# Performance work log

Measured on AMD Instinct MI355X. Metric: run time of the kernel, lower is better.

## Reference

```python
import jax, jax.numpy as jnp
import numpy as np

B, S, E = 4, 2048, 1024
H, D = 16, 64  # num_heads, attention_head_dim


def setup_inputs() -> dict:
    key = jax.random.key(0)
    ks = jax.random.split(key, 9)
    scale_e = 1.0 / np.sqrt(E)
    scale_hd = 1.0 / np.sqrt(H * D)
    x = jax.random.normal(ks[0], (B, S, E), dtype=jnp.float32)
    # per-head projection weights, stacked: [H, E, D]
    Wq = jax.random.uniform(ks[1], (H, E, D), minval=-scale_e, maxval=scale_e, dtype=jnp.float32)
    Wk = jax.random.uniform(ks[2], (H, E, D), minval=-scale_e, maxval=scale_e, dtype=jnp.float32)
    Wv = jax.random.uniform(ks[3], (H, E, D), minval=-scale_e, maxval=scale_e, dtype=jnp.float32)
    bq = jax.random.uniform(ks[4], (H, D), minval=-scale_e, maxval=scale_e, dtype=jnp.float32)
    bk = jax.random.uniform(ks[5], (H, D), minval=-scale_e, maxval=scale_e, dtype=jnp.float32)
    bv = jax.random.uniform(ks[6], (H, D), minval=-scale_e, maxval=scale_e, dtype=jnp.float32)
    Wo = jax.random.uniform(ks[7], (H * D, E), minval=-scale_hd, maxval=scale_hd, dtype=jnp.float32)
    bo = jax.random.uniform(ks[8], (E,), minval=-scale_hd, maxval=scale_hd, dtype=jnp.float32)
    return {"x": x, "Wq": Wq, "Wk": Wk, "Wv": Wv, "bq": bq, "bk": bk, "bv": bv, "Wo": Wo, "bo": bo}


def reference(x, Wq, Wk, Wv, bq, bk, bv, Wo, bo):
    # Per-head QKV projections, vectorized over heads: [B,H,S,D]
    Q = jnp.einsum('bse,hed->bhsd', x, Wq) + bq[None, :, None, :]
    K = jnp.einsum('bse,hed->bhsd', x, Wk) + bk[None, :, None, :]
    V = jnp.einsum('bse,hed->bhsd', x, Wv) + bv[None, :, None, :]
    scale = 1.0 / jnp.sqrt(jnp.asarray(D, dtype=Q.dtype))
    scores = jnp.einsum('bhsd,bhtd->bhst', Q, K) * scale  # [B,H,S,S]
    attn = jax.nn.softmax(scores, axis=-1)
    Z = jnp.einsum('bhst,bhtd->bhsd', attn, V)            # [B,H,S,D]
    # concat heads on feature dim -> [B,S,H*D], then output projection
    Zc = jnp.transpose(Z, (0, 2, 1, 3)).reshape(B, S, H * D)
    return Zc @ Wo + bo
```

## Files before the change

kernel.cpp:

```cpp
#include <hip/hip_runtime.h>


typedef __attribute__((ext_vector_type(4)))  float   f32x4;
typedef __attribute__((ext_vector_type(16))) float   f32x16;
typedef __attribute__((ext_vector_type(8)))  __bf16  bf16x8;
typedef __attribute__((ext_vector_type(4)))  __bf16  bf16x4;
typedef __attribute__((ext_vector_type(4)))  unsigned int u32x4;
typedef unsigned int u32;

#if __has_builtin(__builtin_amdgcn_exp2f)
#define EXP2F(x) __builtin_amdgcn_exp2f(x)
#else
#define EXP2F(x) exp2f(x)
#endif

__device__ __forceinline__ f32x4 fzero4() {
    f32x4 z = {0.f, 0.f, 0.f, 0.f};
    return z;
}
__device__ __forceinline__ f32x16 fzero16() {
    f32x16 z;
#pragma unroll
    for (int i = 0; i < 16; i++) z[i] = 0.f;
    return z;
}

__device__ __forceinline__ u32 cvtpk_bf16(float lo, float hi_) {
    u32 r;
    asm("v_cvt_pk_bf16_f32 %0, %1, %2" : "=v"(r) : "v"(lo), "v"(hi_));
    return r;
}

__device__ __forceinline__ void gload_lds16(const void* g, void* l) {
    __builtin_amdgcn_global_load_lds(
        (const __attribute__((address_space(1))) u32*)g,
        (__attribute__((address_space(3))) u32*)l, 16, 0, 0);
}

__global__ __launch_bounds__(256) void cvt_f32_bf16_4(
    const float* __restrict__ s, __bf16* __restrict__ d, long n) {
    long i = ((long)blockIdx.x * 256 + threadIdx.x) * 4;
    if (i >= n) return;
    float4 v = *(const float4*)(s + i);
    bf16x4 o = { (__bf16)v.x, (__bf16)v.y, (__bf16)v.z, (__bf16)v.w };
    *(bf16x4*)(d + i) = o;
}

__global__ __launch_bounds__(256) void pack_w_t(
    const float* __restrict__ src, __bf16* __restrict__ dst, int R, int C) {
    __shared__ float t[32][33];
    const int z = blockIdx.z;
    src += (size_t)z * R * C;
    dst += (size_t)z * R * C;
    const int r0 = blockIdx.x * 32, c0 = blockIdx.y * 32;
    const int x = threadIdx.x, y = threadIdx.y;
#pragma unroll
    for (int i = 0; i < 4; i++)
        t[y + i * 8][x] = src[(size_t)(r0 + y + i * 8) * C + c0 + x];
    __syncthreads();
#pragma unroll
    for (int i = 0; i < 4; i++)
        dst[(size_t)(c0 + y + i * 8) * R + r0 + x] = (__bf16)t[x][y + i * 8];
}

__global__ __launch_bounds__(256) void pack_bias(
    const float* __restrict__ bq, const float* __restrict__ bk,
    const float* __restrict__ bv, float* __restrict__ bqkv) {
    int n = blockIdx.x * 256 + threadIdx.x;
    if (n >= 3072) return;
    int t = n >> 10, r = n & 1023;
    const float* s = (t == 0) ? bq : (t == 1) ? bk : bv;
    bqkv[n] = s[r];
}

#define GEMM_STAGE(BUF, KOFF)                                                  \
  {                                                                            \
    gload_lds16(A + arow0 * K + (KOFF) + kcol,                                 \
                (char*)As + (BUF) * 16384 + wid * 1024);                       \
    gload_lds16(A + arow1 * K + (KOFF) + kcol,                                 \
                (char*)As + (BUF) * 16384 + 8192 + wid * 1024);                \
    gload_lds16(Bt + brow * K + (KOFF) + kcol,                                 \
                (char*)Bs + (BUF) * 8192 + wid * 1024);                        \
  }

#define GEMM_COMPUTE(BUF)                                                      \
  {                                                                            \
    bf16x8 a[4], b[4];                                                         \
    _Pragma("unroll")                                                          \
    for (int mi = 0; mi < 4; mi++)                                             \
      a[mi] = *(const bf16x8*)&As[(BUF) * 8192 +                               \
                                  (mr * 64 + mi * 16 + l15) * 32 + l4 * 8];    \
    _Pragma("unroll")                                                          \
    for (int ni = 0; ni < 4; ni++)                                             \
      b[ni] = *(const bf16x8*)&Bs[(BUF) * 4096 +                               \
                                  (nc * 64 + ni * 16 + l15) * 32 + l4 * 8];    \
    _Pragma("unroll")                                                          \
    for (int mi = 0; mi < 4; mi++)                                             \
      _Pragma("unroll")                                                        \
      for (int ni = 0; ni < 4; ni++)                                           \
        acc[mi][ni] = __builtin_amdgcn_mfma_f32_16x16x32_bf16(                 \
            a[mi], b[ni], acc[mi][ni], 0, 0, 0);                               \
  }

#define GEMM_PREAMBLE                                                          \
    const int tid  = threadIdx.x;                                              \
    const int lane = tid & 63, wid = tid >> 6;                                 \
    const int mr = wid >> 1, nc = wid & 1;                                     \
    const int l15 = lane & 15, l4 = lane >> 4;                                 \
    const int bn = blockIdx.x, bm = blockIdx.y;                                \
    const long arow0 = (long)bm * 256 + (tid >> 2);                            \
    const long arow1 = arow0 + 128;                                            \
    const long brow  = (long)bn * 128 + (tid >> 2);                            \
    const int  kcol  = (tid & 3) * 8;                                          \
    f32x4 acc[4][4];                                                           \
    _Pragma("unroll")                                                          \
    for (int i = 0; i < 4; i++)                                                \
      _Pragma("unroll")                                                        \
      for (int j = 0; j < 4; j++) acc[i][j] = fzero4();                        \
    GEMM_STAGE(0, 0)                                                           \
    __syncthreads();                                                           \
    int cur = 0;                                                               \
    for (int k0 = 0; k0 < K; k0 += 32, cur ^= 1) {                             \
        if (k0 + 32 < K) GEMM_STAGE(cur ^ 1, k0 + 32)                          \
        GEMM_COMPUTE(cur)                                                      \
        __syncthreads();                                                       \
    }

template <bool F32OUT>
__global__ __launch_bounds__(512) void gemm_bt(
    const __bf16* __restrict__ A, const __bf16* __restrict__ Bt,
    const float* __restrict__ bias, void* __restrict__ Cout,
    int M, int N, int K, int ldc) {
    __shared__ __bf16 As[2 * 256 * 32];
    __shared__ __bf16 Bs[2 * 128 * 32];
    GEMM_PREAMBLE

#pragma unroll
    for (int mi = 0; mi < 4; mi++)
#pragma unroll
        for (int ni = 0; ni < 4; ni++) {
            const int row = bm * 256 + mr * 64 + mi * 16 + l4 * 4;
            const int col = bn * 128 + nc * 64 + ni * 16 + l15;
            const float bv = bias ? bias[col] : 0.f;
#pragma unroll
            for (int r = 0; r < 4; r++) {
                float v = acc[mi][ni][r] + bv;
                if (F32OUT)
                    ((float*)Cout)[(long)(row + r) * ldc + col] = v;
                else
                    ((__bf16*)Cout)[(long)(row + r) * ldc + col] = (__bf16)v;
            }
        }
}

__global__ __launch_bounds__(512) void gemm_qkv(
    const __bf16* __restrict__ A, const __bf16* __restrict__ Bt,
    const float* __restrict__ bias, __bf16* __restrict__ QKV,
    __bf16* __restrict__ VT, int K) {
    __shared__ __bf16 As[2 * 256 * 32];
    __shared__ __bf16 Bs[2 * 128 * 32];
    GEMM_PREAMBLE

    if (bn < 16) {
#pragma unroll
        for (int mi = 0; mi < 4; mi++)
#pragma unroll
            for (int ni = 0; ni < 4; ni++) {
                const int row = bm * 256 + mr * 64 + mi * 16 + l4 * 4;
                const int col = bn * 128 + nc * 64 + ni * 16 + l15;
                const float bv = bias[col];
#pragma unroll
                for (int r = 0; r < 4; r++)
                    QKV[(long)(row + r) * 3072 + col] =
                        (__bf16)(acc[mi][ni][r] + bv);
            }
    } else {
#pragma unroll
        for (int mi = 0; mi < 4; mi++)
#pragma unroll
            for (int ni = 0; ni < 4; ni++) {
                const int row = bm * 256 + mr * 64 + mi * 16 + l4 * 4;
                const int col = bn * 128 + nc * 64 + ni * 16 + l15;
                const float bv = bias[col];
                const int vcol = col - 2048;
                const int h = vcol >> 6, dcol = vcol & 63;
                const int bb = row >> 11, s = row & 2047;
                bf16x4 o;
#pragma unroll
                for (int r = 0; r < 4; r++)
                    o[r] = (__bf16)(acc[mi][ni][r] + bv);
                *(bf16x4*)&VT[((size_t)(bb * 16 + h) * 64 + dcol) * 2048 + s] = o;
            }
    }
}

__global__ __launch_bounds__(256, 4) void attn_fwd(
    const __bf16* __restrict__ QKV, const __bf16* __restrict__ VT,
    __bf16* __restrict__ Z) {
    const int S = 2048, LDQ = 3072;
    const int dd = blockIdx.x;
    const int blk = (dd & 7) * 128 + (dd >> 3);
    const int qt = blk & 15, bh = blk >> 4, b = bh >> 4, h = bh & 15;
    const int tid = threadIdx.x, wid = tid >> 6, lane = tid & 63;
    const int l31 = lane & 31, hi = lane >> 5;

    __shared__ __bf16 smem[16384];

    const __bf16* Qb = QKV + (size_t)b * S * LDQ + h * 64;
    const __bf16* Kb = Qb + 1024;
    const __bf16* Vb = VT + (size_t)bh * 64 * S;
    const int qrow = qt * 128 + wid * 32;

    bf16x8 qf[4];
#pragma unroll
    for (int kk = 0; kk < 4; kk++)
        qf[kk] = *(const bf16x8*)(Qb + (size_t)(qrow + l31) * LDQ + kk * 16 + hi * 8);

    const int f0 = wid * 2, f1 = wid * 2 + 1;
    const int kr0 = (f0 >> 2) * 32 + l31, kc0 = (f0 & 3) * 16 + hi * 8;
    const int kr1 = (f1 >> 2) * 32 + l31, kc1 = (f1 & 3) * 16 + hi * 8;
    const int vr0 = kr0, vs0 = kc0;
    const int vr1 = kr1, vs1 = kc1;
    const int ldst = lane * 16;

    f32x16 o0 = fzero16(), o1 = fzero16();
    float m_r = -1e30f, l_r = 0.f;
    const float csc = 0.18033688011f;

    gload_lds16(Kb + (size_t)kr0 * LDQ + kc0, (char*)smem + f0 * 1024 + ldst);
    gload_lds16(Kb + (size_t)kr1 * LDQ + kc1, (char*)smem + f1 * 1024 + ldst);
    gload_lds16(Vb + (size_t)vr0 * S + vs0,   (char*)smem + 16384 + f0 * 1024 + ldst);
    gload_lds16(Vb + (size_t)vr1 * S + vs1,   (char*)smem + 16384 + f1 * 1024 + ldst);
    asm volatile("s_waitcnt vmcnt(0)" ::: "memory");
    __syncthreads();

    int cur = 0;
    for (int t0 = 0; t0 < S; t0 += 64, cur ^= 1) {
        if (t0 + 64 < S) {
            char* kl = (char*)smem + (cur ^ 1) * 8192;
            char* vl = (char*)smem + 16384 + (cur ^ 1) * 8192;
            gload_lds16(Kb + (size_t)(t0 + 64 + kr0) * LDQ + kc0, kl + f0 * 1024 + ldst);
            gload_lds16(Kb + (size_t)(t0 + 64 + kr1) * LDQ + kc1, kl + f1 * 1024 + ldst);
            gload_lds16(Vb + (size_t)vr0 * S + t0 + 64 + vs0,     vl + f0 * 1024 + ldst);
            gload_lds16(Vb + (size_t)vr1 * S + t0 + 64 + vs1,     vl + f1 * 1024 + ldst);
        }
        const char* kbase = (const char*)smem + cur * 8192;
        const char* vbase = (const char*)smem + 16384 + cur * 8192;

        bf16x8 kf[8];
#pragma unroll
        for (int f = 0; f < 8; f++)
            kf[f] = *(const bf16x8*)(kbase + f * 1024 + ldst);
        f32x16 s0 = fzero16(), s1 = fzero16();
        __builtin_amdgcn_s_setprio(1);
#pragma unroll
        for (int kk = 0; kk < 4; kk++) {
            s0 = __builtin_amdgcn_mfma_f32_32x32x16_bf16(kf[kk],     qf[kk], s0, 0, 0, 0);
            s1 = __builtin_amdgcn_mfma_f32_32x32x16_bf16(kf[4 + kk], qf[kk], s1, 0, 0, 0);
        }
        __builtin_amdgcn_s_setprio(0);

        float mm[16];
#pragma unroll
        for (int i = 0; i < 16; i++) mm[i] = fmaxf(s0[i], s1[i]);
#pragma unroll
        for (int st = 8; st >= 1; st >>= 1)
#pragma unroll
            for (int i = 0; i < st; i++) mm[i] = fmaxf(mm[i], mm[i + st]);
        const float pm = fmaxf(mm[0], __shfl_xor(mm[0], 32));
        if (!__all(pm - m_r <= 64.f)) {
            const float mnew = fmaxf(m_r, pm);
            const float alpha = EXP2F((m_r - mnew) * csc);
            m_r = mnew;
            l_r *= alpha;
#pragma unroll
            for (int i = 0; i < 16; i++) { o0[i] *= alpha; o1[i] *= alpha; }
        }
        const float mc = m_r * csc;
        float ss[16];
#pragma unroll
        for (int i = 0; i < 16; i++) {
            float p0 = EXP2F(s0[i] * csc - mc); s0[i] = p0;
            float p1 = EXP2F(s1[i] * csc - mc); s1[i] = p1;
            ss[i] = p0 + p1;
        }
#pragma unroll
        for (int st = 8; st >= 1; st >>= 1)
#pragma unroll
            for (int i = 0; i < st; i++) ss[i] += ss[i + st];
        l_r += ss[0] + __shfl_xor(ss[0], 32);

        __builtin_amdgcn_s_setprio(1);
#pragma unroll
        for (int kkt = 0; kkt < 4; kkt++) {
            const int r0 = (kkt & 1) * 8;
            u32 w0, w1, w2, w3;
            if (kkt < 2) {
                w0 = cvtpk_bf16(s0[r0],     s0[r0 + 1]);
                w1 = cvtpk_bf16(s0[r0 + 2], s0[r0 + 3]);
                w2 = cvtpk_bf16(s0[r0 + 4], s0[r0 + 5]);
                w3 = cvtpk_bf16(s0[r0 + 6], s0[r0 + 7]);
            } else {
                w0 = cvtpk_bf16(s1[r0],     s1[r0 + 1]);
                w1 = cvtpk_bf16(s1[r0 + 2], s1[r0 + 3]);
                w2 = cvtpk_bf16(s1[r0 + 4], s1[r0 + 5]);
                w3 = cvtpk_bf16(s1[r0 + 6], s1[r0 + 7]);
            }
            asm("v_permlane32_swap_b32 %0, %1" : "+v"(w0), "+v"(w2));
            asm("v_permlane32_swap_b32 %0, %1" : "+v"(w1), "+v"(w3));
            u32x4 pw = {w0, w1, w2, w3};
            bf16x8 pf = __builtin_bit_cast(bf16x8, pw);
            bf16x8 vf0 = *(const bf16x8*)(vbase + kkt * 1024 + ldst);
            bf16x8 vf1 = *(const bf16x8*)(vbase + (4 + kkt) * 1024 + ldst);
            o0 = __builtin_amdgcn_mfma_f32_32x32x16_bf16(vf0, pf, o0, 0, 0, 0);
            o1 = __builtin_amdgcn_mfma_f32_32x32x16_bf16(vf1, pf, o1, 0, 0, 0);
        }
        __builtin_amdgcn_s_setprio(0);

        asm volatile("s_waitcnt vmcnt(0)" ::: "memory");
        __syncthreads();
    }

    const float inv = 1.0f / l_r;
    __bf16 (*Tl)[72] = (__bf16 (*)[72])smem;
    const int trow = wid * 32 + l31;
#pragma unroll
    for (int g = 0; g < 4; g++) {
        bf16x4 t4a, t4b;
#pragma unroll
        for (int j = 0; j < 4; j++) {
            t4a[j] = (__bf16)(o0[4 * g + j] * inv);
            t4b[j] = (__bf16)(o1[4 * g + j] * inv);
        }
        *(bf16x4*)&Tl[trow][g * 8 + hi * 4]      = t4a;
        *(bf16x4*)&Tl[trow][32 + g * 8 + hi * 4] = t4b;
    }
    asm volatile("s_waitcnt lgkmcnt(0)" ::: "memory");
    __builtin_amdgcn_sched_barrier(0);

    const int rr = wid * 32 + (lane >> 1);
    const int ch = (lane & 1) * 32;
#pragma unroll
    for (int i = 0; i < 4; i++) {
        bf16x8 z = *(const bf16x8*)&Tl[rr][ch + i * 8];
        *(bf16x8*)&Z[((size_t)b * S + qt * 128 + rr) * 1024 + h * 64 + ch + i * 8] = z;
    }
}

extern "C" void kernel_launch(void* const* d_in, const int* in_sizes, int n_in,
                              void* d_out, int out_size, void* d_ws, size_t ws_size,
                              hipStream_t stream) {
    const float* x  = (const float*)d_in[0];
    const float* Wq = (const float*)d_in[1];
    const float* Wk = (const float*)d_in[2];
    const float* Wv = (const float*)d_in[3];
    const float* bq = (const float*)d_in[4];
    const float* bk = (const float*)d_in[5];
    const float* bv = (const float*)d_in[6];
    const float* Wo = (const float*)d_in[7];
    const float* bo = (const float*)d_in[8];
    float* out = (float*)d_out;

    char* p = (char*)d_ws;
    __bf16* xb   = (__bf16*)p; p += 8192L * 1024 * 2;
    __bf16* Wqkv = (__bf16*)p; p += 3072L * 1024 * 2;
    float*  bqkv = (float*)p;  p += 3072L * 4;
    __bf16* QKV  = (__bf16*)p; p += 8192L * 3072 * 2;
    __bf16* VTb  = (__bf16*)p; p += 64L * 64 * 2048 * 2;
    __bf16* Zb   = (__bf16*)p; p += 8192L * 1024 * 2;
    __bf16* Wot  = (__bf16*)p; p += 1024L * 1024 * 2;

    cvt_f32_bf16_4<<<8192, 256, 0, stream>>>(x, xb, 8192L * 1024);
    pack_w_t<<<dim3(32, 2, 16), dim3(32, 8), 0, stream>>>(Wq, Wqkv,                1024, 64);
    pack_w_t<<<dim3(32, 2, 16), dim3(32, 8), 0, stream>>>(Wk, Wqkv + 1024L * 1024, 1024, 64);
    pack_w_t<<<dim3(32, 2, 16), dim3(32, 8), 0, stream>>>(Wv, Wqkv + 2048L * 1024, 1024, 64);
    pack_w_t<<<dim3(32, 32, 1), dim3(32, 8), 0, stream>>>(Wo, Wot, 1024, 1024);
    pack_bias<<<12, 256, 0, stream>>>(bq, bk, bv, bqkv);

    gemm_qkv<<<dim3(24, 32), 512, 0, stream>>>(xb, Wqkv, bqkv, QKV, VTb, 1024);
    attn_fwd<<<1024, 256, 0, stream>>>(QKV, VTb, Zb);
    gemm_bt<true><<<dim3(8, 32), 512, 0, stream>>>(Zb, Wot, bo, out,
                                                   8192, 1024, 1024, 1024);
}
```

Measured before the change: 226.3 us.

## Process two query tiles per attention block to reuse K/V tiles

Each attention workgroup now handles 256 query rows (two 128-row sub-tiles A and B) instead of 128, so every K and V tile loaded into LDS and registers serves twice as many queries. The grid is halved to 512 blocks and launch bounds drop to 2 waves per SIMD to make room for the doubled accumulators and Q fragments. This cuts global and LDS traffic per unit of work, but raises register pressure and lowers occupancy and block count, which on a 256-CU part leaves fewer blocks to spread across the device.

```diff
diff --git a/kernel.cpp b/kernel.cpp
--- a/kernel.cpp
+++ b/kernel.cpp
@@ -194,13 +194,96 @@
     }
 }
 
-__global__ __launch_bounds__(256, 4) void attn_fwd(
+#define ATTN_SM_PV(S0, S1, M_R, L_R, O0, O1)                                   \
+  {                                                                            \
+    float mm[16];                                                              \
+    _Pragma("unroll")                                                          \
+    for (int i = 0; i < 16; i++) mm[i] = fmaxf(S0[i], S1[i]);                  \
+    _Pragma("unroll")                                                          \
+    for (int st = 8; st >= 1; st >>= 1)                                        \
+      _Pragma("unroll")                                                        \
+      for (int i = 0; i < st; i++) mm[i] = fmaxf(mm[i], mm[i + st]);           \
+    const float pm = fmaxf(mm[0], __shfl_xor(mm[0], 32));                      \
+    if (!__all(pm - M_R <= 64.f)) {              \
+      const float mnew = fmaxf(M_R, pm);                                       \
+      const float alpha = EXP2F((M_R - mnew) * csc);                           \
+      M_R = mnew;                                                              \
+      L_R *= alpha;                                                            \
+      _Pragma("unroll")                                                        \
+      for (int i = 0; i < 16; i++) { O0[i] *= alpha; O1[i] *= alpha; }         \
+    }                                                                          \
+    const float mc = M_R * csc;                                                \
+    float ss[16];                                                              \
+    _Pragma("unroll")                                                          \
+    for (int i = 0; i < 16; i++) {                                             \
+      float p0 = EXP2F(S0[i] * csc - mc); S0[i] = p0;                          \
+      float p1 = EXP2F(S1[i] * csc - mc); S1[i] = p1;                          \
+      ss[i] = p0 + p1;                                                         \
+    }                                                                          \
+    _Pragma("unroll")                                                          \
+    for (int st = 8; st >= 1; st >>= 1)                                        \
+      _Pragma("unroll")                                                        \
+      for (int i = 0; i < st; i++) ss[i] += ss[i + st];                        \
+    L_R += ss[0] + __shfl_xor(ss[0], 32);                                      \
+    __builtin_amdgcn_s_setprio(1);                                             \
+    _Pragma("unroll")                                                          \
+    for (int kkt = 0; kkt < 4; kkt++) {                                        \
+      const int r0 = (kkt & 1) * 8;                                            \
+      u32 w0, w1, w2, w3;                                                      \
+      if (kkt < 2) {                                                           \
+        w0 = cvtpk_bf16(S0[r0],     S0[r0 + 1]);                               \
+        w1 = cvtpk_bf16(S0[r0 + 2], S0[r0 + 3]);                               \
+        w2 = cvtpk_bf16(S0[r0 + 4], S0[r0 + 5]);                               \
+        w3 = cvtpk_bf16(S0[r0 + 6], S0[r0 + 7]);                               \
+      } else {                                                                 \
+        w0 = cvtpk_bf16(S1[r0],     S1[r0 + 1]);                               \
+        w1 = cvtpk_bf16(S1[r0 + 2], S1[r0 + 3]);                               \
+        w2 = cvtpk_bf16(S1[r0 + 4], S1[r0 + 5]);                               \
+        w3 = cvtpk_bf16(S1[r0 + 6], S1[r0 + 7]);                               \
+      }                                                                        \
+      asm("v_permlane32_swap_b32 %0, %1" : "+v"(w0), "+v"(w2));                \
+      asm("v_permlane32_swap_b32 %0, %1" : "+v"(w1), "+v"(w3));                \
+      u32x4 pw = {w0, w1, w2, w3};                                             \
+      bf16x8 pf = __builtin_bit_cast(bf16x8, pw);                              \
+      O0 = __builtin_amdgcn_mfma_f32_32x32x16_bf16(vf[kkt],     pf, O0, 0, 0, 0); \
+      O1 = __builtin_amdgcn_mfma_f32_32x32x16_bf16(vf[4 + kkt], pf, O1, 0, 0, 0); \
+    }                                                                          \
+    __builtin_amdgcn_s_setprio(0);                                             \
+  }
+
+#define ATTN_EPI(O0, O1, L_R, ROWBASE)                                         \
+  {                                                                            \
+    const float inv = 1.0f / L_R;                                              \
+    _Pragma("unroll")                                                          \
+    for (int g = 0; g < 4; g++) {                                              \
+      bf16x4 t4a, t4b;                                                         \
+      _Pragma("unroll")                                                        \
+      for (int j = 0; j < 4; j++) {                                            \
+        t4a[j] = (__bf16)(O0[4 * g + j] * inv);                                \
+        t4b[j] = (__bf16)(O1[4 * g + j] * inv);                                \
+      }                                                                        \
+      *(bf16x4*)&Tl[trow][g * 8 + hi * 4]      = t4a;                          \
+      *(bf16x4*)&Tl[trow][32 + g * 8 + hi * 4] = t4b;                          \
+    }                                                                          \
+    asm volatile("s_waitcnt lgkmcnt(0)" ::: "memory");                         \
+    __builtin_amdgcn_sched_barrier(0);                                         \
+    _Pragma("unroll")                                                          \
+    for (int i = 0; i < 4; i++) {                                              \
+      bf16x8 z = *(const bf16x8*)&Tl[rr][ch + i * 8];                          \
+      *(bf16x8*)&Z[((size_t)b * S + (ROWBASE) + rr) * 1024 + h * 64 +          \
+                   ch + i * 8] = z;                                            \
+    }                                                                          \
+    asm volatile("s_waitcnt lgkmcnt(0)" ::: "memory");                         \
+    __builtin_amdgcn_sched_barrier(0);                                         \
+  }
+
+__global__ __launch_bounds__(256, 2) void attn_fwd(
     const __bf16* __restrict__ QKV, const __bf16* __restrict__ VT,
     __bf16* __restrict__ Z) {
     const int S = 2048, LDQ = 3072;
     const int dd = blockIdx.x;
-    const int blk = (dd & 7) * 128 + (dd >> 3);
-    const int qt = blk & 15, bh = blk >> 4, b = bh >> 4, h = bh & 15;
+    const int blk = (dd & 7) * 64 + (dd >> 3);
+    const int qt = blk & 7, bh = blk >> 3, b = bh >> 4, h = bh & 15;
     const int tid = threadIdx.x, wid = tid >> 6, lane = tid & 63;
     const int l31 = lane & 31, hi = lane >> 5;
 
@@ -209,12 +292,15 @@
     const __bf16* Qb = QKV + (size_t)b * S * LDQ + h * 64;
     const __bf16* Kb = Qb + 1024;
     const __bf16* Vb = VT + (size_t)bh * 64 * S;
-    const int qrow = qt * 128 + wid * 32;
-
-    bf16x8 qf[4];
-#pragma unroll
-    for (int kk = 0; kk < 4; kk++)
-        qf[kk] = *(const bf16x8*)(Qb + (size_t)(qrow + l31) * LDQ + kk * 16 + hi * 8);
+    const int qrowA = qt * 256 + wid * 32;
+    const int qrowB = qrowA + 128;
+
+    bf16x8 qfA[4], qfB[4];
+#pragma unroll
+    for (int kk = 0; kk < 4; kk++) {
+        qfA[kk] = *(const bf16x8*)(Qb + (size_t)(qrowA + l31) * LDQ + kk * 16 + hi * 8);
+        qfB[kk] = *(const bf16x8*)(Qb + (size_t)(qrowB + l31) * LDQ + kk * 16 + hi * 8);
+    }
 
     const int f0 = wid * 2, f1 = wid * 2 + 1;
     const int kr0 = (f0 >> 2) * 32 + l31, kc0 = (f0 & 3) * 16 + hi * 8;
@@ -223,8 +309,9 @@
     const int vr1 = kr1, vs1 = kc1;
     const int ldst = lane * 16;
 
-    f32x16 o0 = fzero16(), o1 = fzero16();
-    float m_r = -1e30f, l_r = 0.f;
+    f32x16 oA0 = fzero16(), oA1 = fzero16();
+    f32x16 oB0 = fzero16(), oB1 = fzero16();
+    float m_rA = -1e30f, l_rA = 0.f, m_rB = -1e30f, l_rB = 0.f;
     const float csc = 0.18033688011f;
 
     gload_lds16(Kb + (size_t)kr0 * LDQ + kc0, (char*)smem + f0 * 1024 + ldst);
@@ -251,100 +338,39 @@
 #pragma unroll
         for (int f = 0; f < 8; f++)
             kf[f] = *(const bf16x8*)(kbase + f * 1024 + ldst);
-        f32x16 s0 = fzero16(), s1 = fzero16();
+        f32x16 sA0 = fzero16(), sA1 = fzero16();
+        f32x16 sB0 = fzero16(), sB1 = fzero16();
         __builtin_amdgcn_s_setprio(1);
 #pragma unroll
         for (int kk = 0; kk < 4; kk++) {
-            s0 = __builtin_amdgcn_mfma_f32_32x32x16_bf16(kf[kk],     qf[kk], s0, 0, 0, 0);
-            s1 = __builtin_amdgcn_mfma_f32_32x32x16_bf16(kf[4 + kk], qf[kk], s1, 0, 0, 0);
+            sA0 = __builtin_amdgcn_mfma_f32_32x32x16_bf16(kf[kk],     qfA[kk], sA0, 0, 0, 0);
+            sA1 = __builtin_amdgcn_mfma_f32_32x32x16_bf16(kf[4 + kk], qfA[kk], sA1, 0, 0, 0);
+        }
+#pragma unroll
+        for (int kk = 0; kk < 4; kk++) {
+            sB0 = __builtin_amdgcn_mfma_f32_32x32x16_bf16(kf[kk],     qfB[kk], sB0, 0, 0, 0);
+            sB1 = __builtin_amdgcn_mfma_f32_32x32x16_bf16(kf[4 + kk], qfB[kk], sB1, 0, 0, 0);
         }
         __builtin_amdgcn_s_setprio(0);
 
-        float mm[16];
-#pragma unroll
-        for (int i = 0; i < 16; i++) mm[i] = fmaxf(s0[i], s1[i]);
-#pragma unroll
-        for (int st = 8; st >= 1; st >>= 1)
-#pragma unroll
-            for (int i = 0; i < st; i++) mm[i] = fmaxf(mm[i], mm[i + st]);
-        const float pm = fmaxf(mm[0], __shfl_xor(mm[0], 32));
-        if (!__all(pm - m_r <= 64.f)) {
-            const float mnew = fmaxf(m_r, pm);
-            const float alpha = EXP2F((m_r - mnew) * csc);
-            m_r = mnew;
-            l_r *= alpha;
-#pragma unroll
-            for (int i = 0; i < 16; i++) { o0[i] *= alpha; o1[i] *= alpha; }
-        }
-        const float mc = m_r * csc;
-        float ss[16];
-#pragma unroll
-        for (int i = 0; i < 16; i++) {
-            float p0 = EXP2F(s0[i] * csc - mc); s0[i] = p0;
-            float p1 = EXP2F(s1[i] * csc - mc); s1[i] = p1;
-            ss[i] = p0 + p1;
-        }
-#pragma unroll
-        for (int st = 8; st >= 1; st >>= 1)
-#pragma unroll
-            for (int i = 0; i < st; i++) ss[i] += ss[i + st];
-        l_r += ss[0] + __shfl_xor(ss[0], 32);
-
-        __builtin_amdgcn_s_setprio(1);
-#pragma unroll
-        for (int kkt = 0; kkt < 4; kkt++) {
-            const int r0 = (kkt & 1) * 8;
-            u32 w0, w1, w2, w3;
-            if (kkt < 2) {
-                w0 = cvtpk_bf16(s0[r0],     s0[r0 + 1]);
-                w1 = cvtpk_bf16(s0[r0 + 2], s0[r0 + 3]);
-                w2 = cvtpk_bf16(s0[r0 + 4], s0[r0 + 5]);
-                w3 = cvtpk_bf16(s0[r0 + 6], s0[r0 + 7]);
-            } else {
-                w0 = cvtpk_bf16(s1[r0],     s1[r0 + 1]);
-                w1 = cvtpk_bf16(s1[r0 + 2], s1[r0 + 3]);
-                w2 = cvtpk_bf16(s1[r0 + 4], s1[r0 + 5]);
-                w3 = cvtpk_bf16(s1[r0 + 6], s1[r0 + 7]);
-            }
-            asm("v_permlane32_swap_b32 %0, %1" : "+v"(w0), "+v"(w2));
-            asm("v_permlane32_swap_b32 %0, %1" : "+v"(w1), "+v"(w3));
-            u32x4 pw = {w0, w1, w2, w3};
-            bf16x8 pf = __builtin_bit_cast(bf16x8, pw);
-            bf16x8 vf0 = *(const bf16x8*)(vbase + kkt * 1024 + ldst);
-            bf16x8 vf1 = *(const bf16x8*)(vbase + (4 + kkt) * 1024 + ldst);
-            o0 = __builtin_amdgcn_mfma_f32_32x32x16_bf16(vf0, pf, o0, 0, 0, 0);
-            o1 = __builtin_amdgcn_mfma_f32_32x32x16_bf16(vf1, pf, o1, 0, 0, 0);
-        }
-        __builtin_amdgcn_s_setprio(0);
+        bf16x8 vf[8];
+#pragma unroll
+        for (int f = 0; f < 8; f++)
+            vf[f] = *(const bf16x8*)(vbase + f * 1024 + ldst);
+
+        ATTN_SM_PV(sA0, sA1, m_rA, l_rA, oA0, oA1)
+        ATTN_SM_PV(sB0, sB1, m_rB, l_rB, oB0, oB1)
 
         asm volatile("s_waitcnt vmcnt(0)" ::: "memory");
         __syncthreads();
     }
 
-    const float inv = 1.0f / l_r;
     __bf16 (*Tl)[72] = (__bf16 (*)[72])smem;
     const int trow = wid * 32 + l31;
-#pragma unroll
-    for (int g = 0; g < 4; g++) {
-        bf16x4 t4a, t4b;
-#pragma unroll
-        for (int j = 0; j < 4; j++) {
-            t4a[j] = (__bf16)(o0[4 * g + j] * inv);
-            t4b[j] = (__bf16)(o1[4 * g + j] * inv);
-        }
-        *(bf16x4*)&Tl[trow][g * 8 + hi * 4]      = t4a;
-        *(bf16x4*)&Tl[trow][32 + g * 8 + hi * 4] = t4b;
-    }
-    asm volatile("s_waitcnt lgkmcnt(0)" ::: "memory");
-    __builtin_amdgcn_sched_barrier(0);
-
     const int rr = wid * 32 + (lane >> 1);
     const int ch = (lane & 1) * 32;
-#pragma unroll
-    for (int i = 0; i < 4; i++) {
-        bf16x8 z = *(const bf16x8*)&Tl[rr][ch + i * 8];
-        *(bf16x8*)&Z[((size_t)b * S + qt * 128 + rr) * 1024 + h * 64 + ch + i * 8] = z;
-    }
+    ATTN_EPI(oA0, oA1, l_rA, qt * 256)
+    ATTN_EPI(oB0, oB1, l_rB, qt * 256 + 128)
 }
 
 extern "C" void kernel_launch(void* const* d_in, const int* in_sizes, int n_in,
@@ -378,7 +404,7 @@
     pack_bias<<<12, 256, 0, stream>>>(bq, bk, bv, bqkv);
 
     gemm_qkv<<<dim3(24, 32), 512, 0, stream>>>(xb, Wqkv, bqkv, QKV, VTb, 1024);
-    attn_fwd<<<1024, 256, 0, stream>>>(QKV, VTb, Zb);
+    attn_fwd<<<512, 256, 0, stream>>>(QKV, VTb, Zb);
     gemm_bt<true><<<dim3(8, 32), 512, 0, stream>>>(Zb, Wot, bo, out,
                                                    8192, 1024, 1024, 1024);
 }
```

Measured after the change: 220.1 us, median of 2. -2.8%, faster.
